# Optimization experiments

Hardware: AMD Instinct MI355X
Metric: run time of the kernel (lower is better)

## Reference

```python
import jax, jax.numpy as jnp
from jax import lax
import numpy as np

B, L, D = 32, 128, 256


def setup_inputs() -> dict:
    key = jax.random.key(0)
    ks = jax.random.split(key, 5)
    glorot_w = float(np.sqrt(6.0 / (D + D)))
    glorot_g = float(np.sqrt(6.0 / (D + 3)))
    return {
        "x": jax.random.normal(ks[0], (B, L, D), dtype=jnp.float32),
        "Wl": jax.random.uniform(ks[1], (D, D), jnp.float32, -glorot_w, glorot_w),
        "Wr": jax.random.uniform(ks[2], (D, D), jnp.float32, -glorot_w, glorot_w),
        "Wb": jnp.zeros((D,), jnp.float32),
        "Gl": jax.random.uniform(ks[3], (D, 3), jnp.float32, -glorot_g, glorot_g),
        "Gr": jax.random.uniform(ks[4], (D, 3), jnp.float32, -glorot_g, glorot_g),
        "Gb": jnp.zeros((3,), jnp.float32),
    }


def reference(x, Wl, Wr, Wb, Gl, Gr, Gb):
    b, maxlen, d = x.shape
    pos = jnp.arange(maxlen - 1)

    def step(sent, t):
        # sent: (b, maxlen, d). Valid prefix length at this level is maxlen - t.
        left = sent[:, :-1]   # (b, maxlen-1, d)
        right = sent[:, 1:]   # (b, maxlen-1, d)
        central = jnp.tanh(jnp.einsum("bld,de->ble", left, Wl)
                           + jnp.einsum("bld,de->ble", right, Wr) + Wb)
        gates = jax.nn.softmax(jnp.einsum("bld,dg->blg", left, Gl)
                               + jnp.einsum("bld,dg->blg", right, Gr) + Gb, axis=-1)
        nxt = (gates[..., 0:1] * left
               + gates[..., 1:2] * central
               + gates[..., 2:3] * right)
        # only the first (maxlen - t - 1) positions are updated (set_subtensor)
        valid = (pos < (maxlen - t - 1))[None, :, None]
        new_front = jnp.where(valid, nxt, left)
        new_sent = sent.at[:, :-1].set(new_front)
        return new_sent, new_sent

    _, levels = lax.scan(step, x, jnp.arange(maxlen - 1))  # (maxlen-1, b, maxlen, d)
    pyramid = jnp.concatenate([x[None], levels], axis=0)    # (maxlen, b, maxlen, d)

    # Level i has valid length t = maxlen - i; masked max-pool over those positions.
    t_vals = jnp.arange(maxlen, 0, -1)            # (maxlen,)
    mask = jnp.arange(maxlen)[None, :] < t_vals[:, None]  # (maxlen, maxlen)
    neg = jnp.finfo(pyramid.dtype).min
    masked = jnp.where(mask[:, None, :, None], pyramid, neg)
    hierarchy = masked.max(axis=2)                # (maxlen, b, d)
    return jnp.transpose(hierarchy, (1, 0, 2))    # (b, maxlen, d)
```

## Files before the change

kernel.cpp:

```cpp
#include <hip/hip_runtime.h>


#define B_ 32
#define L_ 128
#define D_ 256
#define NTHR 512
#define BUFB 16384
#define GBUF 25088
#define PEX  27136
#define SGB  43520
#define LOG2E 1.4426950408889634f
#define PS_SLOTS 568
#define BROW_U64 131072

typedef _Float16 half8 __attribute__((ext_vector_type(8)));
typedef float f32x4 __attribute__((ext_vector_type(4)));
typedef unsigned u32x4 __attribute__((ext_vector_type(4)));

#define SWZ(o)  ((o) ^ ((((o) >> 9) & 7) << 4))
#define MFMA16 __builtin_amdgcn_mfma_f32_16x16x32_f16
#define LDS_BARRIER() asm volatile("s_waitcnt lgkmcnt(0)\n\ts_barrier" ::: "memory")

#define PIN(H) { \
    u32x4 t_ = __builtin_bit_cast(u32x4, H); \
    unsigned p0_ = t_[0], p1_ = t_[1], p2_ = t_[2], p3_ = t_[3]; \
    asm volatile("" : "+v"(p0_), "+v"(p1_), "+v"(p2_), "+v"(p3_)); \
    t_[0] = p0_; t_[1] = p1_; t_[2] = p2_; t_[3] = p3_; \
    H = __builtin_bit_cast(half8, t_); }

__global__ void prep_wt(const float* __restrict__ Wl, const float* __restrict__ Wr,
                        const float* __restrict__ Gl, const float* __restrict__ Gr,
                        _Float16* __restrict__ WT) {
    int j = blockIdx.x;
    for (int k = threadIdx.x; k < 512; k += 256) {
        float v = 0.f;
        if (j < 256) v = (k < 256) ? Wl[k * 256 + j] : Wr[(k - 256) * 256 + j];
        else { int jj = j - 256; if (jj < 3) v = (k < 256) ? Gl[k * 3 + jj] : Gr[(k - 256) * 3 + jj]; }
        WT[(size_t)j * 512 + k] = (_Float16)v;
    }
}

__global__ void init_misc(int* __restrict__ flags, unsigned long long* __restrict__ brow) {
    int b = blockIdx.x, c = threadIdx.x;
    if (b == 0) for (int i = c; i < 2 * 256 * 16; i += 256) flags[i] = 0;
    for (int i = b * 256 + c; i < BROW_U64; i += 32 * 256) brow[i] = 0ull;
}

__global__ void decode_out(const unsigned* __restrict__ pmax, float* __restrict__ out) {
    const unsigned* pmax0 = pmax + (size_t)32 * PS_SLOTS * 128;
    for (size_t i = (size_t)blockIdx.x * 256 + threadIdx.x; i < (size_t)32 * 128 * 256;
         i += (size_t)gridDim.x * 256) {
        int c = (int)(i & 255);
        int k = (int)((i >> 8) & 127);
        int b = (int)(i / (128 * 256));
        int dw = ((c >> 5) & 1) * 64 + ((c >> 6) & 3) * 16 + (c & 15);
        int hi = (c >> 4) & 1;
        float mx = -3.4e38f;
        if (k == 0) {
            #pragma unroll
            for (int h = 0; h < 8; ++h) {
                unsigned u = pmax0[((size_t)b * 8 + h) * 128 + dw];
                unsigned short us = hi ? (unsigned short)(u >> 16) : (unsigned short)(u & 0xffff);
                mx = fmaxf(mx, (float)__builtin_bit_cast(_Float16, us));
            }
        } else {
            int hcnt = (143 - k) >> 4;
            for (int h = 0; h < hcnt; ++h) {
                int slot = 127 * h - 8 * h * (h - 1) + (k - 1);
                unsigned u = pmax[((size_t)b * PS_SLOTS + slot) * 128 + dw];
                unsigned short us = hi ? (unsigned short)(u >> 16) : (unsigned short)(u & 0xffff);
                mx = fmaxf(mx, (float)__builtin_bit_cast(_Float16, us));
            }
        }
        out[((size_t)b * 128 + k) * 256 + c] = mx;
    }
}

__global__ __launch_bounds__(NTHR, 2) void grcnn_main(
    const float* __restrict__ x, const _Float16* __restrict__ WT,
    const float* __restrict__ Wb, const float* __restrict__ Gb,
    unsigned* __restrict__ pmax, unsigned long long* __restrict__ brow,
    int* __restrict__ flags)
{
    __shared__ alignas(16) char lds[SGB + 1536];

    const int tid = threadIdx.x;
    const int b = blockIdx.x & 31, h = blockIdx.x >> 5;
    const int w = tid >> 6, l = tid & 63, lr = l & 15, q = l >> 4;
    const int g = w & 3, khalf = w >> 2;
    const int cw = g * 64 + khalf * 32;

    const _Float16* wtb0 = WT + (size_t)(64 * g + lr) * 512 + khalf * 256 + q * 8;
    const _Float16* wtb1 = WT + (size_t)(64 * g + 16 + lr) * 512 + khalf * 256 + q * 8;
    const _Float16* wtb2 = WT + (size_t)(64 * g + 32 + lr) * 512 + khalf * 256 + q * 8;
    const _Float16* wtb3 = WT + (size_t)(64 * g + 48 + lr) * 512 + khalf * 256 + q * 8;
#define LDW1(T, i) half8 W##T##_##i = *(const half8*)(wtb##T + i * 32); PIN(W##T##_##i)
#define LDWT(T) LDW1(T,0) LDW1(T,1) LDW1(T,2) LDW1(T,3) LDW1(T,4) LDW1(T,5) LDW1(T,6) LDW1(T,7)
    LDWT(0) LDWT(1) LDWT(2) LDWT(3)
#undef LDWT
#undef LDW1
    const _Float16* wpg = WT + (size_t)(256 + lr) * 512 + q * 8;
    const half8 WG0 = *(const half8*)(wpg + (8 * khalf + 2 * g) * 32);
    const half8 WG1 = *(const half8*)(wpg + (8 * khalf + 2 * g + 1) * 32);

    const float wb0 = Wb[cw + lr], wb1 = Wb[cw + 16 + lr];
    const float gbi0 = Gb[0], gbi1 = Gb[1], gbi2 = Gb[2];

#define RDA(i) const int rd##i = SWZ(lr * 512 + (8 * khalf + i) * 64 + q * 16);
    RDA(0) RDA(1) RDA(2) RDA(3) RDA(4) RDA(5) RDA(6) RDA(7)
#undef RDA
    int wo[2][4];
    #pragma unroll
    for (int nt = 0; nt < 2; ++nt)
        #pragma unroll
        for (int r = 0; r < 4; ++r)
            wo[nt][r] = SWZ((q * 4 + r) * 512 + (cw + nt * 16 + lr) * 2);
    const int impA = 8192 + l * 8;
    const int bnd0 = 8192 + (cw + lr) * 2;
    const int bnd1 = 8192 + (cw + 16 + lr) * 2;
    const int gwo = GBUF + (w * 16 + lr) * 16;
    const int sgw = SGB + w * 192;
#define PSLOT(T) (PEX + (((g * 4 + (T)) * 64 + l) * 16))

    int* ackP  = &flags[(256 + b * 8 + h) * 16];
    int* ackC  = &flags[(256 + b * 8 + h - 1) * 16];
    const int slotbase = 127 * h - 8 * h * (h - 1);
    unsigned* pmax0 = pmax + (size_t)32 * PS_SLOTS * 128;

    for (int ch = tid; ch < 17 * 32; ch += NTHR) {
        int row = ch >> 5, kc = ch & 31;
        int grow = 16 * h + row; if (grow > 127) grow = 127;
        const float* xp = x + ((size_t)b * L_ + grow) * D_ + kc * 8;
        half8 v;
        #pragma unroll
        for (int j = 0; j < 8; ++j) v[j] = (_Float16)xp[j];
        int off = SWZ(row * 512 + kc * 16);
        *(half8*)(lds + off) = v;
        *(half8*)(lds + BUFB + off) = v;
    }
    __syncthreads();

    float cv0[4], cv1[4];
    #pragma unroll
    for (int i = 0; i < 4; ++i) {
        cv0[i] = (float)*(const _Float16*)(lds + SWZ((q * 4 + i) * 512 + (cw + lr) * 2));
        cv1[i] = (float)*(const _Float16*)(lds + SWZ((q * 4 + i) * 512 + (cw + 16 + lr) * 2));
    }

    {
        float c0 = fmaxf(fmaxf(cv0[0], cv0[1]), fmaxf(cv0[2], cv0[3]));
        float c1 = fmaxf(fmaxf(cv1[0], cv1[1]), fmaxf(cv1[2], cv1[3]));
        c0 = fmaxf(c0, __shfl_xor(c0, 16, 64)); c0 = fmaxf(c0, __shfl_xor(c0, 32, 64));
        c1 = fmaxf(c1, __shfl_xor(c1, 16, 64)); c1 = fmaxf(c1, __shfl_xor(c1, 32, 64));
        if (l < 16) {
            unsigned ph = (unsigned)__builtin_bit_cast(unsigned short, (_Float16)c0)
                        | ((unsigned)__builtin_bit_cast(unsigned short, (_Float16)c1) << 16);
            pmax0[((size_t)b * 8 + h) * 128 + w * 16 + l] = ph;
        }
    }

    int rb = 0;

    for (int t = 0; t < 127; ++t) {
        const int m = 127 - t - 16 * h;
        if (m <= 0) break;
        const int mm = (m > 16) ? 16 : m;
        const bool doExpN = (h >= 1) && (126 - t >= 16 * h);
        const bool doImpT = (h < 7) && (t <= 110 - 16 * h);
        const int rw = rb ^ BUFB;

        f32x4 p0 = {}, p1 = {}, p2 = {}, p3 = {}, ag = {};
#define STEP(i) { \
            half8 av = *(const half8*)(lds + (rd##i ^ rb)); \
            p0 = MFMA16(av, W0_##i, p0, 0, 0, 0); \
            p1 = MFMA16(av, W1_##i, p1, 0, 0, 0); \
            p2 = MFMA16(av, W2_##i, p2, 0, 0, 0); \
            p3 = MFMA16(av, W3_##i, p3, 0, 0, 0); \
            if ((i >> 1) == g) \
                ag = MFMA16((i & 1) ? WG1 : WG0, av, ag, 0, 0, 0); }
        STEP(0) STEP(1) STEP(2) STEP(3) STEP(4) STEP(5) STEP(6) STEP(7)
#undef STEP

        if (khalf == 0) {
            *(f32x4*)(lds + PSLOT(2)) = p2;
            *(f32x4*)(lds + PSLOT(3)) = p3;
        } else {
            *(f32x4*)(lds + PSLOT(0)) = p0;
            *(f32x4*)(lds + PSLOT(1)) = p1;
        }
        if (l < 16) *(f32x4*)(lds + gwo) = ag;

        LDS_BARRIER();

        f32x4 a0, a1;
        if (khalf == 0) {
            a0 = p0 + *(const f32x4*)(lds + PSLOT(0));
            a1 = p1 + *(const f32x4*)(lds + PSLOT(1));
        } else {
            a0 = p2 + *(const f32x4*)(lds + PSLOT(2));
            a1 = p3 + *(const f32x4*)(lds + PSLOT(3));
        }

        if (l < 16) {
            float s0g = gbi0, s1g = gbi1, s2g = gbi2;
            #pragma unroll
            for (int w8 = 0; w8 < 8; ++w8) {
                f32x4 v = *(const f32x4*)(lds + GBUF + (w8 * 16 + l) * 16);
                s0g += v[0]; s1g += v[1]; s2g += v[2];
            }
            float mg = fmaxf(fmaxf(s0g, s1g), s2g);
            float ee0 = __builtin_amdgcn_exp2f((s0g - mg) * LOG2E);
            float ee1 = __builtin_amdgcn_exp2f((s1g - mg) * LOG2E);
            float ee2 = __builtin_amdgcn_exp2f((s2g - mg) * LOG2E);
            float inv = __builtin_amdgcn_rcpf(ee0 + ee1 + ee2);
            float* sp = (float*)(lds + sgw + l * 12);
            sp[0] = ee0 * inv; sp[1] = ee1 * inv; sp[2] = ee2 * inv;
        }
        asm volatile("s_waitcnt lgkmcnt(0)" ::: "memory");
        __builtin_amdgcn_sched_barrier(0);
        f32x4 v0 = *(const f32x4*)(lds + sgw + q * 48);
        f32x4 v1 = *(const f32x4*)(lds + sgw + q * 48 + 16);
        f32x4 v2 = *(const f32x4*)(lds + sgw + q * 48 + 32);
        float g0a[4] = { v0[0], v0[3], v1[2], v2[1] };
        float g1a[4] = { v0[1], v1[0], v1[3], v2[2] };
        float g2a[4] = { v0[2], v1[1], v2[0], v2[3] };

        float b0 = (float)*(const _Float16*)(lds + (bnd0 ^ rb));
        float b1 = (float)*(const _Float16*)(lds + (bnd1 ^ rb));
        float s0 = __shfl(cv0[0], (l + 16) & 63, 64);
        float s1 = __shfl(cv1[0], (l + 16) & 63, 64);

        if (doExpN && t >= 3 && l == 0) {
            while (__hip_atomic_load(ackC, __ATOMIC_RELAXED, __HIP_MEMORY_SCOPE_AGENT) < t - 3)
                __builtin_amdgcn_s_sleep(1);
        }

        const unsigned long long tagv = (unsigned long long)(t + 1) << 32;
        float cm0 = -3.4e38f, cm1 = -3.4e38f;
        #pragma unroll
        for (int r = 0; r < 4; ++r) {
            const int row = q * 4 + r;
            float g0f = g0a[r];
            float g1f = g1a[r];
            float g2f = g2a[r];
            if (row < mm) {
                #define EPI(NT, ACC, CV, SHV, BV, WBV, CMV) {                                \
                    float pre = ACC[r] + WBV;                                                \
                    float exx = __builtin_amdgcn_exp2f(pre * (2.f * LOG2E));                 \
                    float ce = 1.f - 2.f * __builtin_amdgcn_rcpf(exx + 1.f);                 \
                    float lv = CV[r];                                                        \
                    float rv = (r < 3) ? CV[(r < 3) ? r + 1 : 0] : (q < 3 ? SHV : BV);       \
                    float nx = g0f * lv + g1f * ce + g2f * rv;                               \
                    CMV = fmaxf(CMV, nx);                                                    \
                    _Float16 nh = (_Float16)nx;                                              \
                    CV[r] = nx;                       \
                    int pdi = __builtin_amdgcn_update_dpp(                                   \
                        0, __builtin_bit_cast(int, nx), 0xB1, 0xF, 0xF, true);               \
                    float pnx = __builtin_bit_cast(float, pdi);                              \
                    unsigned pk = (unsigned)__builtin_bit_cast(unsigned short, nh)           \
                        | ((unsigned)__builtin_bit_cast(unsigned short, (_Float16)pnx) << 16);\
                    if (!(lr & 1)) {                                                         \
                        *(unsigned*)(lds + (wo[NT][r] ^ rw)) = pk;                           \
                        if (r == 0 && q == 0 && doExpN) {                                    \
                            unsigned long long* ep = brow +                                  \
                                (((size_t)((t + 1) & 3) * 32 + b) * 8 + h) * 128             \
                                + (cw >> 1) + NT * 8 + (lr >> 1);                            \
                            __hip_atomic_store(ep, (unsigned long long)pk | tagv,            \
                                               __ATOMIC_RELAXED, __HIP_MEMORY_SCOPE_AGENT);  \
                        }                                                                    \
                    }                                                                        \
                }
                EPI(0, a0, cv0, s0, b0, wb0, cm0)
                EPI(1, a1, cv1, s1, b1, wb1, cm1)
                #undef EPI
            }
        }

        unsigned long long g0v = 0, g1v = 0;
        const unsigned long long* bp = nullptr;
        if (w == 0 && doImpT) {
            bp = brow + (((size_t)((t + 1) & 3) * 32 + b) * 8 + (h + 1)) * 128 + 2 * l;
            g0v = __hip_atomic_load(bp,     __ATOMIC_RELAXED, __HIP_MEMORY_SCOPE_AGENT);
            g1v = __hip_atomic_load(bp + 1, __ATOMIC_RELAXED, __HIP_MEMORY_SCOPE_AGENT);
        }

        cm0 = fmaxf(cm0, __shfl_xor(cm0, 16, 64));
        cm0 = fmaxf(cm0, __shfl_xor(cm0, 32, 64));
        cm1 = fmaxf(cm1, __shfl_xor(cm1, 16, 64));
        cm1 = fmaxf(cm1, __shfl_xor(cm1, 32, 64));
        if (l < 16) {
            unsigned ph = (unsigned)__builtin_bit_cast(unsigned short, (_Float16)cm0)
                        | ((unsigned)__builtin_bit_cast(unsigned short, (_Float16)cm1) << 16);
            pmax[((size_t)b * PS_SLOTS + slotbase + t) * 128 + w * 16 + l] = ph;
        }

        if (w == 0 && doImpT) {
            const unsigned tag = (unsigned)(t + 1);
            while ((unsigned)(g0v >> 32) != tag) {
                __builtin_amdgcn_s_sleep(1);
                g0v = __hip_atomic_load(bp, __ATOMIC_RELAXED, __HIP_MEMORY_SCOPE_AGENT);
            }
            while ((unsigned)(g1v >> 32) != tag) {
                __builtin_amdgcn_s_sleep(1);
                g1v = __hip_atomic_load(bp + 1, __ATOMIC_RELAXED, __HIP_MEMORY_SCOPE_AGENT);
            }
            unsigned long long data = (g0v & 0xffffffffull) | (g1v << 32);
            *(unsigned long long*)(lds + (impA ^ rw)) = data;
            if (l == 0)
                __hip_atomic_store(ackP, t + 1, __ATOMIC_RELAXED, __HIP_MEMORY_SCOPE_AGENT);
        }

        LDS_BARRIER();
        rb ^= BUFB;
    }
}

extern "C" void kernel_launch(void* const* d_in, const int* in_sizes, int n_in,
                              void* d_out, int out_size, void* d_ws, size_t ws_size,
                              hipStream_t stream) {
    const float* x  = (const float*)d_in[0];
    const float* Wl = (const float*)d_in[1];
    const float* Wr = (const float*)d_in[2];
    const float* Wb = (const float*)d_in[3];
    const float* Gl = (const float*)d_in[4];
    const float* Gr = (const float*)d_in[5];
    const float* Gb = (const float*)d_in[6];
    float* out = (float*)d_out;
    char* ws = (char*)d_ws;

    _Float16* WT = (_Float16*)ws;
    unsigned long long* brow = (unsigned long long*)(ws + 278528);
    int* flags = (int*)(ws + 1327104);
    unsigned* pmax = (unsigned*)(ws + 1359872);

    prep_wt<<<272, 256, 0, stream>>>(Wl, Wr, Gl, Gr, WT);
    init_misc<<<B_, 256, 0, stream>>>(flags, brow);

    void* args[] = { (void*)&x, (void*)&WT, (void*)&Wb, (void*)&Gb,
                     (void*)&pmax, (void*)&brow, (void*)&flags };
    hipLaunchCooperativeKernel((const void*)grcnn_main, dim3(B_ * 8), dim3(NTHR),
                               args, 0, stream);

    decode_out<<<1024, 256, 0, stream>>>(pmax, out);
}
```

Before: 371.6 us.

## Give each wave full K reduction to drop cross-wave partial-sum exchange

Changes the work split so each of the 8 waves owns 32 output columns across the full 512-wide K dimension, instead of splitting K in halves between wave pairs. This removes the per-step LDS exchange of partial sums, the extra barrier, and the 8-way reduction of gate partials. Gate weights move into LDS and every wave computes the full gate logits redundantly. The trade is more MFMAs per wave for the gate (16 instead of 2), extra LDS reads of gate weights, and a reshaped output column mapping in the decode kernel.

```diff
diff --git a/kernel.cpp b/kernel.cpp
--- a/kernel.cpp
+++ b/kernel.cpp
@@ -6,9 +6,8 @@
 #define D_ 256
 #define NTHR 512
 #define BUFB 16384
-#define GBUF 25088
-#define PEX  27136
-#define SGB  43520
+#define SGB  9216
+#define GWT  25088
 #define LOG2E 1.4426950408889634f
 #define PS_SLOTS 568
 #define BROW_U64 131072
@@ -53,7 +52,7 @@
         int c = (int)(i & 255);
         int k = (int)((i >> 8) & 127);
         int b = (int)(i / (128 * 256));
-        int dw = ((c >> 5) & 1) * 64 + ((c >> 6) & 3) * 16 + (c & 15);
+        int dw = ((c >> 5) * 16) + (c & 15);
         int hi = (c >> 4) & 1;
         float mx = -3.4e38f;
         if (k == 0) {
@@ -82,32 +81,29 @@
     unsigned* __restrict__ pmax, unsigned long long* __restrict__ brow,
     int* __restrict__ flags)
 {
-    __shared__ alignas(16) char lds[SGB + 1536];
+    __shared__ alignas(16) char lds[GWT + 16384];
 
     const int tid = threadIdx.x;
     const int b = blockIdx.x & 31, h = blockIdx.x >> 5;
     const int w = tid >> 6, l = tid & 63, lr = l & 15, q = l >> 4;
-    const int g = w & 3, khalf = w >> 2;
-    const int cw = g * 64 + khalf * 32;
-
-    const _Float16* wtb0 = WT + (size_t)(64 * g + lr) * 512 + khalf * 256 + q * 8;
-    const _Float16* wtb1 = WT + (size_t)(64 * g + 16 + lr) * 512 + khalf * 256 + q * 8;
-    const _Float16* wtb2 = WT + (size_t)(64 * g + 32 + lr) * 512 + khalf * 256 + q * 8;
-    const _Float16* wtb3 = WT + (size_t)(64 * g + 48 + lr) * 512 + khalf * 256 + q * 8;
-#define LDW1(T, i) half8 W##T##_##i = *(const half8*)(wtb##T + i * 32); PIN(W##T##_##i)
-#define LDWT(T) LDW1(T,0) LDW1(T,1) LDW1(T,2) LDW1(T,3) LDW1(T,4) LDW1(T,5) LDW1(T,6) LDW1(T,7)
-    LDWT(0) LDWT(1) LDWT(2) LDWT(3)
-#undef LDWT
-#undef LDW1
-    const _Float16* wpg = WT + (size_t)(256 + lr) * 512 + q * 8;
-    const half8 WG0 = *(const half8*)(wpg + (8 * khalf + 2 * g) * 32);
-    const half8 WG1 = *(const half8*)(wpg + (8 * khalf + 2 * g + 1) * 32);
+    const int cw = w * 32;
+
+    const _Float16* wp0 = WT + (size_t)(cw + lr) * 512 + q * 8;
+    const _Float16* wp1 = WT + (size_t)(cw + 16 + lr) * 512 + q * 8;
+#define LDW(s) \
+    half8 WA##s = *(const half8*)(wp0 + s * 32); \
+    half8 WB##s = *(const half8*)(wp1 + s * 32); \
+    PIN(WA##s) PIN(WB##s)
+    LDW(0) LDW(1) LDW(2) LDW(3) LDW(4) LDW(5) LDW(6) LDW(7)
+    LDW(8) LDW(9) LDW(10) LDW(11) LDW(12) LDW(13) LDW(14) LDW(15)
+#undef LDW
 
     const float wb0 = Wb[cw + lr], wb1 = Wb[cw + 16 + lr];
     const float gbi0 = Gb[0], gbi1 = Gb[1], gbi2 = Gb[2];
 
-#define RDA(i) const int rd##i = SWZ(lr * 512 + (8 * khalf + i) * 64 + q * 16);
+#define RDA(i) const int rd##i = SWZ(lr * 512 + i * 64 + q * 16);
     RDA(0) RDA(1) RDA(2) RDA(3) RDA(4) RDA(5) RDA(6) RDA(7)
+    RDA(8) RDA(9) RDA(10) RDA(11) RDA(12) RDA(13) RDA(14) RDA(15)
 #undef RDA
     int wo[2][4];
     #pragma unroll
@@ -118,15 +114,20 @@
     const int impA = 8192 + l * 8;
     const int bnd0 = 8192 + (cw + lr) * 2;
     const int bnd1 = 8192 + (cw + 16 + lr) * 2;
-    const int gwo = GBUF + (w * 16 + lr) * 16;
     const int sgw = SGB + w * 192;
-#define PSLOT(T) (PEX + (((g * 4 + (T)) * 64 + l) * 16))
+    const int gva = GWT + (l << 4);
 
     int* ackP  = &flags[(256 + b * 8 + h) * 16];
     int* ackC  = &flags[(256 + b * 8 + h - 1) * 16];
     const int slotbase = 127 * h - 8 * h * (h - 1);
     unsigned* pmax0 = pmax + (size_t)32 * PS_SLOTS * 128;
 
+    for (int ch = tid; ch < 1024; ch += NTHR) {
+        int i = ch >> 6, ll = ch & 63;
+        int llr = ll & 15, lq = ll >> 4;
+        half8 v = *(const half8*)(WT + (size_t)(256 + llr) * 512 + i * 32 + lq * 8);
+        *(half8*)(lds + GWT + ch * 16) = v;
+    }
     for (int ch = tid; ch < 17 * 32; ch += NTHR) {
         int row = ch >> 5, kc = ch & 31;
         int grow = 16 * h + row; if (grow > 127) grow = 127;
@@ -169,49 +170,23 @@
         const bool doImpT = (h < 7) && (t <= 110 - 16 * h);
         const int rw = rb ^ BUFB;
 
-        f32x4 p0 = {}, p1 = {}, p2 = {}, p3 = {}, ag = {};
+        f32x4 a0 = {}, a1 = {}, ag = {};
 #define STEP(i) { \
             half8 av = *(const half8*)(lds + (rd##i ^ rb)); \
-            p0 = MFMA16(av, W0_##i, p0, 0, 0, 0); \
-            p1 = MFMA16(av, W1_##i, p1, 0, 0, 0); \
-            p2 = MFMA16(av, W2_##i, p2, 0, 0, 0); \
-            p3 = MFMA16(av, W3_##i, p3, 0, 0, 0); \
-            if ((i >> 1) == g) \
-                ag = MFMA16((i & 1) ? WG1 : WG0, av, ag, 0, 0, 0); }
+            half8 gv = *(const half8*)(lds + gva + i * 1024); \
+            a0 = MFMA16(av, WA##i, a0, 0, 0, 0); \
+            a1 = MFMA16(av, WB##i, a1, 0, 0, 0); \
+            ag = MFMA16(gv, av, ag, 0, 0, 0); }
         STEP(0) STEP(1) STEP(2) STEP(3) STEP(4) STEP(5) STEP(6) STEP(7)
+        STEP(8) STEP(9) STEP(10) STEP(11) STEP(12) STEP(13) STEP(14) STEP(15)
 #undef STEP
 
-        if (khalf == 0) {
-            *(f32x4*)(lds + PSLOT(2)) = p2;
-            *(f32x4*)(lds + PSLOT(3)) = p3;
-        } else {
-            *(f32x4*)(lds + PSLOT(0)) = p0;
-            *(f32x4*)(lds + PSLOT(1)) = p1;
-        }
-        if (l < 16) *(f32x4*)(lds + gwo) = ag;
-
-        LDS_BARRIER();
-
-        f32x4 a0, a1;
-        if (khalf == 0) {
-            a0 = p0 + *(const f32x4*)(lds + PSLOT(0));
-            a1 = p1 + *(const f32x4*)(lds + PSLOT(1));
-        } else {
-            a0 = p2 + *(const f32x4*)(lds + PSLOT(2));
-            a1 = p3 + *(const f32x4*)(lds + PSLOT(3));
-        }
-
         if (l < 16) {
-            float s0g = gbi0, s1g = gbi1, s2g = gbi2;
-            #pragma unroll
-            for (int w8 = 0; w8 < 8; ++w8) {
-                f32x4 v = *(const f32x4*)(lds + GBUF + (w8 * 16 + l) * 16);
-                s0g += v[0]; s1g += v[1]; s2g += v[2];
-            }
-            float mg = fmaxf(fmaxf(s0g, s1g), s2g);
-            float ee0 = __builtin_amdgcn_exp2f((s0g - mg) * LOG2E);
-            float ee1 = __builtin_amdgcn_exp2f((s1g - mg) * LOG2E);
-            float ee2 = __builtin_amdgcn_exp2f((s2g - mg) * LOG2E);
+            float p0 = ag[0] + gbi0, p1 = ag[1] + gbi1, p2 = ag[2] + gbi2;
+            float mg = fmaxf(fmaxf(p0, p1), p2);
+            float ee0 = __builtin_amdgcn_exp2f((p0 - mg) * LOG2E);
+            float ee1 = __builtin_amdgcn_exp2f((p1 - mg) * LOG2E);
+            float ee2 = __builtin_amdgcn_exp2f((p2 - mg) * LOG2E);
             float inv = __builtin_amdgcn_rcpf(ee0 + ee1 + ee2);
             float* sp = (float*)(lds + sgw + l * 12);
             sp[0] = ee0 * inv; sp[1] = ee1 * inv; sp[2] = ee2 * inv;
```

Result: faster. 331.8 us (-10.7%).
